# Optimization experiments

Measured on AMD Instinct MI355X. Metric: run time of the kernel, lower is better.

The kernel has to match this reference:

```python
import jax, jax.numpy as jnp
import numpy as np

NA = 5            # num_anchors
NC = 13           # num_classes
COORD_SCALE = 1.0
NOOBJ_SCALE = 1.0
OBJ_SCALE = 5.0
# corner_confidence9 constants (singleshotpose defaults)
TH = 80.0
SHARP = 2.0
IMW = 640.0
IMH = 480.0


def _forward(output, target):
    nB, _, nH, nW = output.shape
    out = output.reshape(nB, NA, 19 + NC, nH, nW)
    # channels 0,1 sigmoided in-place in the torch code; 2..17 raw
    xys_pred = jnp.concatenate([jax.nn.sigmoid(out[:, :, 0:2]), out[:, :, 2:18]], axis=2)  # [nB,nA,18,nH,nW]
    conf = jax.nn.sigmoid(out[:, :, 18])  # [nB,nA,nH,nW]

    # --- build_targets (done on output.data / target.data in torch -> stop_gradient) ---
    pc = jax.lax.stop_gradient(xys_pred)
    gxr = jnp.arange(nW, dtype=pc.dtype)
    gyr = jnp.arange(nH, dtype=pc.dtype)
    px = (pc[:, :, 0::2] + gxr[None, None, None, None, :]) / nW  # [nB,nA,9,nH,nW] normalized x corners
    py = (pc[:, :, 1::2] + gyr[None, None, None, :, None]) / nH  # [nB,nA,9,nH,nW] normalized y corners

    tgt = jax.lax.stop_gradient(target).reshape(nB, 50, 21)
    coords = tgt[:, :, 1:19]  # [nB,50,18] normalized gt corners (x0,y0,...,x8,y8)
    # torch loop breaks at first zero x0 -> prefix-valid mask
    valid = jnp.cumprod((coords[:, :, 0] != 0).astype(jnp.int32), axis=1).astype(bool)
    gi = jnp.floor(coords[:, :, 0] * nW).astype(jnp.int32)  # [nB,50]
    gj = jnp.floor(coords[:, :, 1] * nH).astype(jnp.int32)

    b_idx = jnp.broadcast_to(jnp.arange(nB)[:, None], (nB, 50))
    # predicted box at assigned cell, anchor best_n = 0 (as in source)
    prx = px[b_idx, 0, :, gj, gi]  # [nB,50,9]
    pry = py[b_idx, 0, :, gj, gi]
    pbox = jnp.stack([prx, pry], axis=-1).reshape(nB, 50, 18)

    # corner_confidence9 (singleshotpose): mean of thresholded exp-distance conf over 9 corners
    d = (coords - pbox).reshape(nB, 50, 9, 2) * jnp.array([IMW, IMH], dtype=coords.dtype)
    dn = jnp.sqrt(jnp.sum(d * d, axis=-1))  # [nB,50,9] pixel distances
    cvals = (jnp.exp(SHARP * (1.0 - dn / TH)) - 1.0) * (dn < TH).astype(coords.dtype)
    conf_t = jnp.mean(cvals, axis=-1) / (jnp.exp(jnp.asarray(SHARP, coords.dtype)) - 1.0 + 1e-5)  # [nB,50]

    # route invalid targets out of bounds -> dropped by scatter
    gi_s = jnp.where(valid, gi, nW)
    gj_s = jnp.where(valid, gj, nH)
    bf = b_idx.reshape(-1)
    gif = gi_s.reshape(-1)
    gjf = gj_s.reshape(-1)

    coord_mask = jnp.zeros((nB, NA, nH, nW), output.dtype).at[bf, 0, gjf, gif].set(1.0)
    conf_mask = jnp.full((nB, NA, nH, nW), NOOBJ_SCALE, output.dtype).at[bf, 0, gjf, gif].set(OBJ_SCALE)
    tconf = jnp.zeros((nB, NA, nH, nW), output.dtype).at[bf, 0, gjf, gif].set(conf_t.reshape(-1))

    tx = coords[:, :, 0::2] * nW - gi[..., None].astype(coords.dtype)  # [nB,50,9]
    ty = coords[:, :, 1::2] * nH - gj[..., None].astype(coords.dtype)
    tvals = jnp.stack([tx, ty], axis=-1).reshape(nB * 50, 18)
    tar = jnp.zeros((nB, NA, 18, nH, nW), output.dtype).at[bf, 0, :, gjf, gif].set(tvals)

    # --- losses ---
    cm = coord_mask[:, :, None]  # [nB,nA,1,nH,nW]
    loss_xy = COORD_SCALE * jnp.sum((xys_pred * cm - tar * cm) ** 2) / 2.0
    cms = jnp.sqrt(conf_mask)
    loss_conf = jnp.sum((conf * cms - tconf * cms) ** 2) / 2.0
    return loss_xy + loss_conf


def setup_inputs() -> dict:
    key = jax.random.key(0)
    k1, k2 = jax.random.split(key)
    output = jax.random.normal(k1, (32, NA * (19 + NC), 76, 76), dtype=jnp.float32)
    target = jax.random.uniform(k2, (32, 50 * 21), dtype=jnp.float32)
    return {"output": output, "target": target}


def reference(output, target):
    return _forward(output, target)
```

## Files before the change

kernel.cpp:

```cpp
#include <hip/hip_runtime.h>
#include <math.h>

#define NB 32
#define NA 5
#define NC 13
#define NHH 76
#define NWW 76
#define NT 50
#define CH (19 + NC)
#define CELLS (NHH * NWW)
#define NBA (NB * NA)
#define V4_PER_SLAB (CELLS / 4)
#define TOTAL_V4 (NBA * V4_PER_SLAB)
#define SWEEP_BLOCKS 512
#define GRID_BLOCKS (SWEEP_BLOCKS + NB)
#define NPART GRID_BLOCKS

#define OBJ_SCALE 5.0f
#define TH_ 80.0f
#define SHARP_ 2.0f
#define IMW_ 640.0f
#define IMH_ 480.0f

__device__ __forceinline__ float sigmoidf_(float x) {
    return 1.0f / (1.0f + expf(-x));
}

__global__ void main_kernel(const float* __restrict__ outp,
                            const float* __restrict__ tgt,
                            double* __restrict__ partials) {
    int bid = blockIdx.x;
    int tid = threadIdx.x;

    if (bid < SWEEP_BLOCKS) {
        double acc = 0.0;
        for (int idx = bid * 256 + tid; idx < TOTAL_V4; idx += SWEEP_BLOCKS * 256) {
            int ba = idx / V4_PER_SLAB;
            int r  = idx - ba * V4_PER_SLAB;
            const float4* slab =
                (const float4*)(outp + ((size_t)ba * CH + 18) * CELLS);
            float4 q = slab[r];
            float a0 = sigmoidf_(q.x), a1 = sigmoidf_(q.y);
            float a2 = sigmoidf_(q.z), a3 = sigmoidf_(q.w);
            acc += 0.5 * (double)(a0 * a0 + a1 * a1 + a2 * a2 + a3 * a3);
        }
        __shared__ double sdata[256];
        sdata[tid] = acc;
        __syncthreads();
        for (int s = 128; s > 0; s >>= 1) {
            if (tid < s) sdata[tid] += sdata[tid + s];
            __syncthreads();
        }
        if (tid == 0) partials[bid] = sdata[0];
    } else {
        int b = bid - SWEEP_BLOCKS;
        __shared__ int sgi[NT], sgj[NT], snz[NT], svalid[NT];

        if (tid < NT) {
            const float* tg = tgt + (size_t)(b * NT + tid) * 21;
            float cx = tg[1];
            float cy = tg[2];
            sgi[tid] = (int)floorf(cx * (float)NWW);
            sgj[tid] = (int)floorf(cy * (float)NHH);
            snz[tid] = (cx != 0.0f) ? 1 : 0;
        }
        __syncthreads();
        if (tid < NT) {
            int v = 1;
            for (int k = 0; k <= tid; ++k) v &= snz[k];
            svalid[tid] = v;
        }
        __syncthreads();

        double local = 0.0;
        if (tid < NT) {
            int gi = sgi[tid], gj = sgj[tid];
            bool inb = (gi >= 0 && gi < NWW && gj >= 0 && gj < NHH);
            bool win = svalid[tid] && inb;
            if (win) {
                for (int k2 = tid + 1; k2 < NT; ++k2) {
                    if (svalid[k2] && sgi[k2] == gi && sgj[k2] == gj) { win = false; break; }
                }
            }
            if (win) {
                const float* tg = tgt + (size_t)(b * NT + tid) * 21;
                int cell = gj * NWW + gi;
                const float* base = outp + (size_t)b * NA * CH * CELLS;

                float v[19];
                #pragma unroll
                for (int c = 0; c < 19; ++c) v[c] = base[(size_t)c * CELLS + cell];
                float s0 = sigmoidf_(v[0]);
                float s1 = sigmoidf_(v[1]);
                float confv = sigmoidf_(v[18]);

                const float denom = expf(SHARP_) - 1.0f + 1e-5f;
                float ssum = 0.0f;
                #pragma unroll
                for (int k = 0; k < 9; ++k) {
                    float vx = (k == 0) ? s0 : v[2 * k];
                    float vy = (k == 0) ? s1 : v[2 * k + 1];
                    float px = (vx + (float)gi) / (float)NWW;
                    float py = (vy + (float)gj) / (float)NHH;
                    float dx = (tg[1 + 2 * k] - px) * IMW_;
                    float dy = (tg[2 + 2 * k] - py) * IMH_;
                    float dn = sqrtf(dx * dx + dy * dy);
                    if (dn < TH_) ssum += expf(SHARP_ * (1.0f - dn / TH_)) - 1.0f;
                }
                float conf_t = (ssum / 9.0f) / denom;

                float cs = 0.0f;
                #pragma unroll
                for (int k = 0; k < 9; ++k) {
                    float tvx = tg[1 + 2 * k] * (float)NWW - (float)gi;
                    float tvy = tg[2 + 2 * k] * (float)NHH - (float)gj;
                    float dx = ((k == 0) ? s0 : v[2 * k]) - tvx;
                    float dy = ((k == 0) ? s1 : v[2 * k + 1]) - tvy;
                    cs += dx * dx + dy * dy;
                }

                float dc = confv - conf_t;
                local = 0.5 * (double)(OBJ_SCALE * dc * dc - confv * confv + cs);
            }
        }

        __shared__ double sdata2[256];
        sdata2[tid] = local;
        __syncthreads();
        for (int s = 128; s > 0; s >>= 1) {
            if (tid < s) sdata2[tid] += sdata2[tid + s];
            __syncthreads();
        }
        if (tid == 0) partials[bid] = sdata2[0];
    }
}

__global__ void final_kernel(const double* __restrict__ partials,
                             float* __restrict__ out) {
    __shared__ double sdata[256];
    double acc = 0.0;
    for (int i = threadIdx.x; i < NPART; i += 256) acc += partials[i];
    sdata[threadIdx.x] = acc;
    __syncthreads();
    for (int s = 128; s > 0; s >>= 1) {
        if (threadIdx.x < s) sdata[threadIdx.x] += sdata[threadIdx.x + s];
        __syncthreads();
    }
    if (threadIdx.x == 0) out[0] = (float)sdata[0];
}

extern "C" void kernel_launch(void* const* d_in, const int* in_sizes, int n_in,
                              void* d_out, int out_size, void* d_ws, size_t ws_size,
                              hipStream_t stream) {
    const float* outp = (const float*)d_in[0];
    const float* tgt  = (const float*)d_in[1];
    float* out = (float*)d_out;
    double* partials = (double*)d_ws;

    main_kernel<<<GRID_BLOCKS, 256, 0, stream>>>(outp, tgt, partials);
    final_kernel<<<1, 256, 0, stream>>>(partials, out);
}
```

Baseline: 20.25 us.

## Replace two-kernel reduction with float atomicAdd and fewer sweep blocks

Drops the separate final reduction kernel. Each block now atomically adds its float partial into the output, which is zeroed by a memset on the same stream. The sweep grid also shrinks from 512 to 192 blocks, giving each thread more work and fewer atomics. The cost is a memset node plus float atomics whose summation order is nondeterministic and loses the double-precision final accumulation.

```diff
diff --git a/kernel.cpp b/kernel.cpp
--- a/kernel.cpp
+++ b/kernel.cpp
@@ -12,9 +12,8 @@
 #define NBA (NB * NA)
 #define V4_PER_SLAB (CELLS / 4)
 #define TOTAL_V4 (NBA * V4_PER_SLAB)
-#define SWEEP_BLOCKS 512
+#define SWEEP_BLOCKS 192
 #define GRID_BLOCKS (SWEEP_BLOCKS + NB)
-#define NPART GRID_BLOCKS
 
 #define OBJ_SCALE 5.0f
 #define TH_ 80.0f
@@ -28,12 +27,12 @@
 
 __global__ void main_kernel(const float* __restrict__ outp,
                             const float* __restrict__ tgt,
-                            double* __restrict__ partials) {
+                            float* __restrict__ out) {
     int bid = blockIdx.x;
     int tid = threadIdx.x;
+    double local = 0.0;
 
     if (bid < SWEEP_BLOCKS) {
-        double acc = 0.0;
         for (int idx = bid * 256 + tid; idx < TOTAL_V4; idx += SWEEP_BLOCKS * 256) {
             int ba = idx / V4_PER_SLAB;
             int r  = idx - ba * V4_PER_SLAB;
@@ -42,16 +41,8 @@
             float4 q = slab[r];
             float a0 = sigmoidf_(q.x), a1 = sigmoidf_(q.y);
             float a2 = sigmoidf_(q.z), a3 = sigmoidf_(q.w);
-            acc += 0.5 * (double)(a0 * a0 + a1 * a1 + a2 * a2 + a3 * a3);
+            local += 0.5 * (double)(a0 * a0 + a1 * a1 + a2 * a2 + a3 * a3);
         }
-        __shared__ double sdata[256];
-        sdata[tid] = acc;
-        __syncthreads();
-        for (int s = 128; s > 0; s >>= 1) {
-            if (tid < s) sdata[tid] += sdata[tid + s];
-            __syncthreads();
-        }
-        if (tid == 0) partials[bid] = sdata[0];
     } else {
         int b = bid - SWEEP_BLOCKS;
         __shared__ int sgi[NT], sgj[NT], snz[NT], svalid[NT];
@@ -72,7 +63,6 @@
         }
         __syncthreads();
 
-        double local = 0.0;
         if (tid < NT) {
             int gi = sgi[tid], gj = sgj[tid];
             bool inb = (gi >= 0 && gi < NWW && gj >= 0 && gj < NHH);
@@ -123,30 +113,16 @@
                 local = 0.5 * (double)(OBJ_SCALE * dc * dc - confv * confv + cs);
             }
         }
+    }
 
-        __shared__ double sdata2[256];
-        sdata2[tid] = local;
-        __syncthreads();
-        for (int s = 128; s > 0; s >>= 1) {
-            if (tid < s) sdata2[tid] += sdata2[tid + s];
-            __syncthreads();
-        }
-        if (tid == 0) partials[bid] = sdata2[0];
-    }
-}
-
-__global__ void final_kernel(const double* __restrict__ partials,
-                             float* __restrict__ out) {
     __shared__ double sdata[256];
-    double acc = 0.0;
-    for (int i = threadIdx.x; i < NPART; i += 256) acc += partials[i];
-    sdata[threadIdx.x] = acc;
+    sdata[tid] = local;
     __syncthreads();
     for (int s = 128; s > 0; s >>= 1) {
-        if (threadIdx.x < s) sdata[threadIdx.x] += sdata[threadIdx.x + s];
+        if (tid < s) sdata[tid] += sdata[tid + s];
         __syncthreads();
     }
-    if (threadIdx.x == 0) out[0] = (float)sdata[0];
+    if (tid == 0) atomicAdd(out, (float)sdata[0]);
 }
 
 extern "C" void kernel_launch(void* const* d_in, const int* in_sizes, int n_in,
@@ -155,8 +131,7 @@
     const float* outp = (const float*)d_in[0];
     const float* tgt  = (const float*)d_in[1];
     float* out = (float*)d_out;
-    double* partials = (double*)d_ws;
 
-    main_kernel<<<GRID_BLOCKS, 256, 0, stream>>>(outp, tgt, partials);
-    final_kernel<<<1, 256, 0, stream>>>(partials, out);
+    hipMemsetAsync(out, 0, sizeof(float), stream);
+    main_kernel<<<GRID_BLOCKS, 256, 0, stream>>>(outp, tgt, out);
 }
```

Result: slower. 22.44 us (+10.8%).
